# Kernel tuning notes

Measured on AMD Instinct MI355X. Metric: run time of the kernel, lower is better.

The kernel has to match this reference:

```python
import jax, jax.numpy as jnp
import numpy as np

COST_CLASS, COST_MASK, COST_DICE = 2.0, 5.0, 5.0
NUM_POINTS = 12544

def setup_inputs() -> dict:
    key = jax.random.key(0)
    k1, k2, k3, k4, k5 = jax.random.split(key, 5)
    bs, Q, K = 4, 100, 134
    H = W = 256
    M = 80
    P = H * W
    pred_logits = jax.random.normal(k1, (bs, Q, K), dtype=jnp.float32)
    pred_masks = jax.random.normal(k2, (bs, Q, H, W), dtype=jnp.float32)
    tgt_labels = jax.random.randint(k3, (M,), 0, K - 1, dtype=jnp.int32)
    # binary target masks, stored as float (matches .float() in torch code)
    tgt_masks = (jax.random.uniform(k4, (M, H, W)) > 0.5).astype(jnp.float32)
    # random subset of points without replacement (torch.randperm[:num_points])
    point_idx = jax.random.permutation(k5, P)[:NUM_POINTS].astype(jnp.int32)
    return {"pred_logits": pred_logits, "pred_masks": pred_masks,
            "tgt_labels": tgt_labels, "tgt_masks": tgt_masks,
            "point_idx": point_idx}

def reference(pred_logits, pred_masks, tgt_labels, tgt_masks, point_idx):
    bs, Q, K = pred_logits.shape
    N = bs * Q
    M = tgt_masks.shape[0]
    Pn = point_idx.shape[0]

    # class cost: -p[n, tgt_id[m]]
    out_prob = jax.nn.softmax(pred_logits.reshape(N, K), axis=-1)
    tgt_ids = jnp.clip(tgt_labels.astype(jnp.int32), 0, K - 1)
    cost_class = -out_prob[:, tgt_ids]                      # (N, M)

    # sampled mask logits / targets
    x = pred_masks.reshape(N, -1)[:, point_idx]             # (N, Pn) logits
    y = tgt_masks.reshape(M, -1)[:, point_idx]              # (M, Pn) binary float

    # BCE-with-logits cost, separable form:
    # mean_p[softplus(x) - x*y] = mean_p softplus(x) - (x @ y^T)/Pn
    sp_mean = jnp.mean(jax.nn.softplus(x), axis=-1)         # (N,)
    xy = jnp.einsum('np,mp->nm', x, y)                      # (N, M)
    cost_mask = sp_mean[:, None] - xy / Pn

    # dice cost
    s = jax.nn.sigmoid(x)                                   # (N, Pn)
    numer = 2.0 * jnp.einsum('np,mp->nm', s, y)             # (N, M)
    denom = jnp.sum(s, axis=-1)[:, None] + jnp.sum(y, axis=-1)[None, :]
    cost_dice = 1.0 - (numer + 1.0) / (denom + 1.0)

    C = COST_CLASS * cost_class + COST_MASK * cost_mask + COST_DICE * cost_dice
    return C.reshape(bs, Q, M)
```

## Files before the change

### kernel.cpp

```cpp
#include <hip/hip_runtime.h>
#include <math.h>

#define N_ROWS 400
#define M_ROWS 80
#define K_CLS  134
#define PN     12544
#define PFULL  65536
#define NSUB   25
#define TSTEPS 392
#define KSPLIT 98
#define TPB    4

#define GY_BLOCKS 245
#define SM_BLOCKS 50

typedef __attribute__((ext_vector_type(4))) float  f32x4;
typedef __attribute__((ext_vector_type(8))) __bf16 bf16x8;

__device__ __forceinline__ float wave_reduce_sum(float v) {
#pragma unroll
    for (int off = 32; off > 0; off >>= 1) v += __shfl_down(v, off, 64);
    return v;
}

__global__ __launch_bounds__(1024) void sel_sort_kernel(
        const int* __restrict__ point_idx, int* __restrict__ sel,
        float* __restrict__ zero_region, int zero_n) {
    __shared__ unsigned int flagw[PFULL / 4];
    __shared__ int wtot[16], wbase[16];
    int tid = threadIdx.x;
    for (int i = tid; i < PFULL / 4; i += 1024) flagw[i] = 0u;
    for (int i = tid; i < zero_n; i += 1024) zero_region[i] = 0.f;
    __syncthreads();
    unsigned char* flag = (unsigned char*)flagw;
    for (int i = tid; i < PN; i += 1024) flag[point_idx[i]] = 1;
    __syncthreads();
    unsigned int w[16];
    int cnt = 0;
#pragma unroll
    for (int j = 0; j < 16; ++j) {
        w[j] = flagw[tid * 16 + j];
        cnt += (int)((w[j] * 0x01010101u) >> 24);
    }
    int lane = tid & 63, wid = tid >> 6;
    int v = cnt;
#pragma unroll
    for (int off = 1; off < 64; off <<= 1) {
        int u = __shfl_up(v, off, 64);
        if (lane >= off) v += u;
    }
    if (lane == 63) wtot[wid] = v;
    __syncthreads();
    if (tid == 0) {
        int run = 0;
#pragma unroll
        for (int i = 0; i < 16; ++i) { wbase[i] = run; run += wtot[i]; }
    }
    __syncthreads();
    int base = wbase[wid] + (v - cnt);
#pragma unroll
    for (int j = 0; j < 16; ++j) {
        unsigned int u = w[j];
        int p0 = tid * 64 + j * 4;
        if (u & 0x01u)       sel[base++] = p0;
        if (u & 0x0100u)     sel[base++] = p0 + 1;
        if (u & 0x010000u)   sel[base++] = p0 + 2;
        if (u & 0x01000000u) sel[base++] = p0 + 3;
    }
}

__global__ __launch_bounds__(512) void stage1b_kernel(
        const float* __restrict__ tgt_masks, const float* __restrict__ pred_logits,
        const int* __restrict__ sel, __bf16* __restrict__ Yb,
        float* __restrict__ ysum, float* __restrict__ rowmax, float* __restrict__ rowsum) {
    __shared__ float smem[128];
    int b = blockIdx.x;
    if (b < GY_BLOCKS) {
        int j = b / 49, tch = b % 49;
        int wave = threadIdx.x >> 6, lane = threadIdx.x & 63;
        int colL = lane & 15, quad = lane >> 4;
        int m = 16 * j + colL;
        int t = tch * 8 + wave;
        int k0 = t * 32 + quad * 8;
        const float* yrow = tgt_masks + (size_t)m * PFULL;
        int idx[8];
        *(int4*)(idx)     = *(const int4*)(sel + k0);
        *(int4*)(idx + 4) = *(const int4*)(sel + k0 + 4);
        bf16x8 v; float acc = 0.f;
#pragma unroll
        for (int jj = 0; jj < 8; ++jj) {
            float y = yrow[idx[jj]];
            v[jj] = (__bf16)y;
            acc += y;
        }
        ((bf16x8*)Yb)[(size_t)(t * 5 + j) * 64 + lane] = v;
        acc += __shfl_down(acc, 32, 64);
        acc += __shfl_down(acc, 16, 64);
        if (quad == 0) smem[wave * 16 + colL] = acc;
        __syncthreads();
        if (threadIdx.x < 16) {
            float s = 0.f;
#pragma unroll
            for (int wv = 0; wv < 8; ++wv) s += smem[wv * 16 + threadIdx.x];
            atomicAdd(&ysum[16 * j + threadIdx.x], s);
        }
    } else {
        int bb = b - GY_BLOCKS;
        int wave = threadIdx.x >> 6, lane = threadIdx.x & 63;
        int n = bb * 8 + wave;
        const float* row = pred_logits + n * K_CLS;
        float mx = -1e30f;
        for (int k = lane; k < K_CLS; k += 64) mx = fmaxf(mx, row[k]);
#pragma unroll
        for (int off = 32; off > 0; off >>= 1) mx = fmaxf(mx, __shfl_down(mx, off, 64));
        mx = __shfl(mx, 0, 64);
        float se = 0.f;
        for (int k = lane; k < K_CLS; k += 64) se += expf(row[k] - mx);
        se = wave_reduce_sum(se);
        if (lane == 0) { rowmax[n] = mx; rowsum[n] = se; }
    }
}

__global__ __launch_bounds__(256) void gemm_fused_kernel(
        const float* __restrict__ pred_masks, const int* __restrict__ sel,
        const __bf16* __restrict__ Yb,
        float* __restrict__ xyacc, float* __restrict__ syacc,
        float* __restrict__ spsum, float* __restrict__ ssum) {
    int wave = threadIdx.x >> 6, lane = threadIdx.x & 63;
    int flat = blockIdx.x * 4 + wave;
    if (flat >= NSUB * KSPLIT) return;
    int nsub = flat / KSPLIT, kc = flat % KSPLIT;
    int n0 = nsub * 16;
    int colL = lane & 15, quad = lane >> 4;
    int tbase = kc * TPB;

    const float* row = pred_masks + (size_t)(n0 + colL) * PFULL;
    const bf16x8* Yfrag = (const bf16x8*)Yb;

    f32x4 accX[5], accS[5];
    f32x4 zero = {0.f, 0.f, 0.f, 0.f};
#pragma unroll
    for (int j = 0; j < 5; ++j) { accX[j] = zero; accS[j] = zero; }
    float sumS = 0.f, sumSP = 0.f;

    float xs[2][8];
    bf16x8 Bbuf[2][5];
    auto load = [&](int i, int b) {
        int t = tbase + i;
        int k0 = t * 32 + quad * 8;
        int idx[8];
        *(int4*)(idx)     = *(const int4*)(sel + k0);
        *(int4*)(idx + 4) = *(const int4*)(sel + k0 + 4);
#pragma unroll
        for (int jj = 0; jj < 8; ++jj) xs[b][jj] = row[idx[jj]];
        const bf16x8* q = Yfrag + (size_t)(t * 5) * 64 + lane;
#pragma unroll
        for (int j = 0; j < 5; ++j) Bbuf[b][j] = q[(size_t)j * 64];
    };
    auto process = [&](int b) {
        bf16x8 aX, aS;
#pragma unroll
        for (int jj = 0; jj < 8; ++jj) {
            float x  = xs[b][jj];
            float ax = fabsf(x);
            float e  = __expf(-ax);
            float inv = __builtin_amdgcn_rcpf(1.f + e);
            float sig = (x >= 0.f) ? inv : e * inv;
            float sp  = fmaxf(x, 0.f) + __logf(1.f + e);
            aX[jj] = (__bf16)x; aS[jj] = (__bf16)sig;
            sumS += sig; sumSP += sp;
        }
#pragma unroll
        for (int j = 0; j < 5; ++j) {
            accX[j] = __builtin_amdgcn_mfma_f32_16x16x32_bf16(aX, Bbuf[b][j], accX[j], 0, 0, 0);
            accS[j] = __builtin_amdgcn_mfma_f32_16x16x32_bf16(aS, Bbuf[b][j], accS[j], 0, 0, 0);
        }
    };

    load(0, 0);
#pragma unroll
    for (int i = 0; i < TPB; ++i) {
        int b = i & 1;
        if (i + 1 < TPB) load(i + 1, b ^ 1);
        process(b);
    }

#pragma unroll
    for (int j = 0; j < 5; ++j)
#pragma unroll
        for (int r = 0; r < 4; ++r) {
            int n = n0 + quad * 4 + r;
            int m = 16 * j + colL;
            atomicAdd(&xyacc[n * M_ROWS + m], accX[j][r]);
            atomicAdd(&syacc[n * M_ROWS + m], accS[j][r]);
        }
    sumS  += __shfl_down(sumS, 32, 64);
    sumS  += __shfl_down(sumS, 16, 64);
    sumSP += __shfl_down(sumSP, 32, 64);
    sumSP += __shfl_down(sumSP, 16, 64);
    if (lane < 16) {
        atomicAdd(&ssum[n0 + lane], sumS);
        atomicAdd(&spsum[n0 + lane], sumSP);
    }
}

__global__ void combine_kernel(const float* __restrict__ logits,
                               const int* __restrict__ tgt_labels,
                               const float* __restrict__ rowmax,
                               const float* __restrict__ rowsum,
                               const float* __restrict__ spsum,
                               const float* __restrict__ ssum,
                               const float* __restrict__ ysum,
                               const float* __restrict__ xyacc,
                               const float* __restrict__ syacc,
                               float* __restrict__ out) {
    int idx = blockIdx.x * blockDim.x + threadIdx.x;
    if (idx >= N_ROWS * M_ROWS) return;
    int n = idx / M_ROWS, m = idx % M_ROWS;
    int tid = tgt_labels[m];
    tid = min(max(tid, 0), K_CLS - 1);
    float p = expf(logits[n * K_CLS + tid] - rowmax[n]) / rowsum[n];
    float cost_class = -p;
    float cost_mask = (spsum[n] - xyacc[idx]) * (1.0f / PN);
    float cost_dice = 1.f - (2.f * syacc[idx] + 1.f) / (ssum[n] + ysum[m] + 1.f);
    out[idx] = 2.f * cost_class + 5.f * cost_mask + 5.f * cost_dice;
}

extern "C" void kernel_launch(void* const* d_in, const int* in_sizes, int n_in,
                              void* d_out, int out_size, void* d_ws, size_t ws_size,
                              hipStream_t stream) {
    const float* pred_logits = (const float*)d_in[0];
    const float* pred_masks  = (const float*)d_in[1];
    const int*   tgt_labels  = (const int*)d_in[2];
    const float* tgt_masks   = (const float*)d_in[3];
    const int*   point_idx   = (const int*)d_in[4];
    float* out = (float*)d_out;

    char* ws = (char*)d_ws;
    size_t off = 0;
    auto carve = [&](size_t nbytes) {
        char* p = ws + off;
        off += (nbytes + 255) & ~(size_t)255;
        return p;
    };
    float* xyacc = (float*)carve((size_t)N_ROWS * M_ROWS * 4);
    float* syacc = (float*)carve((size_t)N_ROWS * M_ROWS * 4);
    float* ysum  = (float*)carve(M_ROWS * 4);
    float* spsum = (float*)carve(N_ROWS * 4);
    float* ssum  = (float*)carve(N_ROWS * 4);
    int zero_n = (int)(off / 4);
    int*   sel    = (int*)carve(PN * 4);
    float* rowmax = (float*)carve(N_ROWS * 4);
    float* rowsum = (float*)carve(N_ROWS * 4);
    __bf16* Yb = (__bf16*)carve((size_t)TSTEPS * 5 * 1024);
    (void)ws_size; (void)in_sizes; (void)n_in; (void)out_size;

    sel_sort_kernel<<<1, 1024, 0, stream>>>(point_idx, sel, xyacc, zero_n);
    stage1b_kernel<<<GY_BLOCKS + SM_BLOCKS, 512, 0, stream>>>(
        tgt_masks, pred_logits, sel, Yb, ysum, rowmax, rowsum);
    int nwaves = NSUB * KSPLIT;
    gemm_fused_kernel<<<(nwaves + 3) / 4, 256, 0, stream>>>(
        pred_masks, sel, Yb, xyacc, syacc, spsum, ssum);
    combine_kernel<<<(N_ROWS * M_ROWS + 255) / 256, 256, 0, stream>>>(
        pred_logits, tgt_labels, rowmax, rowsum, spsum, ssum, ysum, xyacc, syacc, out);
}
```

Before: 217.7 us.

## Rebalance stages: bitmask sort with softmax, parallel zeroing, finer GEMM K-split

The single-block sort kernel now builds a 65536-bit bitmask with atomicOr and emits indices via popcount/ctz. Softmax row stats move into this launch as extra blocks. Workspace zeroing moves out of the one-block kernel into dedicated vectorized blocks of the gather stage, and per-chunk target sums are written without atomics and summed in the combine kernel. The GEMM K-split doubles to 196 chunks of 2 steps with all loads issued up front. This gives more waves and shorter serial work, at the cost of twice as many output atomics.

```diff
diff --git a/kernel.cpp b/kernel.cpp
--- a/kernel.cpp
+++ b/kernel.cpp
@@ -8,11 +8,11 @@
 #define PFULL  65536
 #define NSUB   25
 #define TSTEPS 392
-#define KSPLIT 98
-#define TPB    4
-
+#define KSPLIT 196
+#define TPB    2
+
+#define ZB_BLOCKS 33
 #define GY_BLOCKS 245
-#define SM_BLOCKS 50
 
 typedef __attribute__((ext_vector_type(4))) float  f32x4;
 typedef __attribute__((ext_vector_type(8))) __bf16 bf16x8;
@@ -23,91 +23,46 @@
     return v;
 }
 
-__global__ __launch_bounds__(1024) void sel_sort_kernel(
+__global__ __launch_bounds__(1024) void sort_softmax_kernel(
         const int* __restrict__ point_idx, int* __restrict__ sel,
-        float* __restrict__ zero_region, int zero_n) {
-    __shared__ unsigned int flagw[PFULL / 4];
-    __shared__ int wtot[16], wbase[16];
+        const float* __restrict__ pred_logits,
+        float* __restrict__ rowmax, float* __restrict__ rowsum) {
     int tid = threadIdx.x;
-    for (int i = tid; i < PFULL / 4; i += 1024) flagw[i] = 0u;
-    for (int i = tid; i < zero_n; i += 1024) zero_region[i] = 0.f;
-    __syncthreads();
-    unsigned char* flag = (unsigned char*)flagw;
-    for (int i = tid; i < PN; i += 1024) flag[point_idx[i]] = 1;
-    __syncthreads();
-    unsigned int w[16];
-    int cnt = 0;
-#pragma unroll
-    for (int j = 0; j < 16; ++j) {
-        w[j] = flagw[tid * 16 + j];
-        cnt += (int)((w[j] * 0x01010101u) >> 24);
-    }
-    int lane = tid & 63, wid = tid >> 6;
-    int v = cnt;
-#pragma unroll
-    for (int off = 1; off < 64; off <<= 1) {
-        int u = __shfl_up(v, off, 64);
-        if (lane >= off) v += u;
-    }
-    if (lane == 63) wtot[wid] = v;
-    __syncthreads();
-    if (tid == 0) {
-        int run = 0;
-#pragma unroll
-        for (int i = 0; i < 16; ++i) { wbase[i] = run; run += wtot[i]; }
-    }
-    __syncthreads();
-    int base = wbase[wid] + (v - cnt);
-#pragma unroll
-    for (int j = 0; j < 16; ++j) {
-        unsigned int u = w[j];
-        int p0 = tid * 64 + j * 4;
-        if (u & 0x01u)       sel[base++] = p0;
-        if (u & 0x0100u)     sel[base++] = p0 + 1;
-        if (u & 0x010000u)   sel[base++] = p0 + 2;
-        if (u & 0x01000000u) sel[base++] = p0 + 3;
-    }
-}
-
-__global__ __launch_bounds__(512) void stage1b_kernel(
-        const float* __restrict__ tgt_masks, const float* __restrict__ pred_logits,
-        const int* __restrict__ sel, __bf16* __restrict__ Yb,
-        float* __restrict__ ysum, float* __restrict__ rowmax, float* __restrict__ rowsum) {
-    __shared__ float smem[128];
-    int b = blockIdx.x;
-    if (b < GY_BLOCKS) {
-        int j = b / 49, tch = b % 49;
-        int wave = threadIdx.x >> 6, lane = threadIdx.x & 63;
-        int colL = lane & 15, quad = lane >> 4;
-        int m = 16 * j + colL;
-        int t = tch * 8 + wave;
-        int k0 = t * 32 + quad * 8;
-        const float* yrow = tgt_masks + (size_t)m * PFULL;
-        int idx[8];
-        *(int4*)(idx)     = *(const int4*)(sel + k0);
-        *(int4*)(idx + 4) = *(const int4*)(sel + k0 + 4);
-        bf16x8 v; float acc = 0.f;
-#pragma unroll
-        for (int jj = 0; jj < 8; ++jj) {
-            float y = yrow[idx[jj]];
-            v[jj] = (__bf16)y;
-            acc += y;
-        }
-        ((bf16x8*)Yb)[(size_t)(t * 5 + j) * 64 + lane] = v;
-        acc += __shfl_down(acc, 32, 64);
-        acc += __shfl_down(acc, 16, 64);
-        if (quad == 0) smem[wave * 16 + colL] = acc;
-        __syncthreads();
-        if (threadIdx.x < 16) {
-            float s = 0.f;
-#pragma unroll
-            for (int wv = 0; wv < 8; ++wv) s += smem[wv * 16 + threadIdx.x];
-            atomicAdd(&ysum[16 * j + threadIdx.x], s);
-        }
+    if (blockIdx.x == 0) {
+        __shared__ unsigned int bits[PFULL / 32];
+        __shared__ int wtot[16], wbase[16];
+        bits[tid] = 0u; bits[tid + 1024] = 0u;
+        __syncthreads();
+        for (int i = tid; i < PN; i += 1024) {
+            int p = point_idx[i];
+            atomicOr(&bits[p >> 5], 1u << (p & 31));
+        }
+        __syncthreads();
+        unsigned int w0 = bits[tid * 2], w1 = bits[tid * 2 + 1];
+        int cnt = __popc(w0) + __popc(w1);
+        int lane = tid & 63, wid = tid >> 6;
+        int v = cnt;
+#pragma unroll
+        for (int off = 1; off < 64; off <<= 1) {
+            int u = __shfl_up(v, off, 64);
+            if (lane >= off) v += u;
+        }
+        if (lane == 63) wtot[wid] = v;
+        __syncthreads();
+        if (tid == 0) {
+            int run = 0;
+#pragma unroll
+            for (int i = 0; i < 16; ++i) { wbase[i] = run; run += wtot[i]; }
+        }
+        __syncthreads();
+        int base = wbase[wid] + (v - cnt);
+        int p0 = tid * 64;
+        while (w0) { int b = __builtin_ctz(w0); w0 &= w0 - 1; sel[base++] = p0 + b; }
+        p0 += 32;
+        while (w1) { int b = __builtin_ctz(w1); w1 &= w1 - 1; sel[base++] = p0 + b; }
     } else {
-        int bb = b - GY_BLOCKS;
-        int wave = threadIdx.x >> 6, lane = threadIdx.x & 63;
-        int n = bb * 8 + wave;
+        int wave = tid >> 6, lane = tid & 63;
+        int n = (blockIdx.x - 1) * 16 + wave;
         const float* row = pred_logits + n * K_CLS;
         float mx = -1e30f;
         for (int k = lane; k < K_CLS; k += 64) mx = fmaxf(mx, row[k]);
@@ -118,6 +73,51 @@
         for (int k = lane; k < K_CLS; k += 64) se += expf(row[k] - mx);
         se = wave_reduce_sum(se);
         if (lane == 0) { rowmax[n] = mx; rowsum[n] = se; }
+    }
+}
+
+__global__ __launch_bounds__(512) void stage1b_kernel(
+        const float* __restrict__ tgt_masks, const int* __restrict__ sel,
+        __bf16* __restrict__ Yb, float* __restrict__ ypart,
+        float* __restrict__ zero_region, int zero_n4) {
+    __shared__ float smem[128];
+    int b = blockIdx.x;
+    if (b < ZB_BLOCKS) {
+        int i = b * 512 + threadIdx.x;
+        if (i < zero_n4) {
+            f32x4 z = {0.f, 0.f, 0.f, 0.f};
+            ((f32x4*)zero_region)[i] = z;
+        }
+        return;
+    }
+    int bb = b - ZB_BLOCKS;
+    int j = bb / 49, tch = bb % 49;
+    int wave = threadIdx.x >> 6, lane = threadIdx.x & 63;
+    int colL = lane & 15, quad = lane >> 4;
+    int m = 16 * j + colL;
+    int t = tch * 8 + wave;
+    int k0 = t * 32 + quad * 8;
+    const float* yrow = tgt_masks + (size_t)m * PFULL;
+    int idx[8];
+    *(int4*)(idx)     = *(const int4*)(sel + k0);
+    *(int4*)(idx + 4) = *(const int4*)(sel + k0 + 4);
+    bf16x8 v; float acc = 0.f;
+#pragma unroll
+    for (int jj = 0; jj < 8; ++jj) {
+        float y = yrow[idx[jj]];
+        v[jj] = (__bf16)y;
+        acc += y;
+    }
+    ((bf16x8*)Yb)[(size_t)(t * 5 + j) * 64 + lane] = v;
+    acc += __shfl_down(acc, 32, 64);
+    acc += __shfl_down(acc, 16, 64);
+    if (quad == 0) smem[wave * 16 + colL] = acc;
+    __syncthreads();
+    if (threadIdx.x < 16) {
+        float s = 0.f;
+#pragma unroll
+        for (int wv = 0; wv < 8; ++wv) s += smem[wv * 16 + threadIdx.x];
+        ypart[tch * M_ROWS + 16 * j + threadIdx.x] = s;
     }
 }
 
@@ -128,7 +128,6 @@
         float* __restrict__ spsum, float* __restrict__ ssum) {
     int wave = threadIdx.x >> 6, lane = threadIdx.x & 63;
     int flat = blockIdx.x * 4 + wave;
-    if (flat >= NSUB * KSPLIT) return;
     int nsub = flat / KSPLIT, kc = flat % KSPLIT;
     int n0 = nsub * 16;
     int colL = lane & 15, quad = lane >> 4;
@@ -143,25 +142,27 @@
     for (int j = 0; j < 5; ++j) { accX[j] = zero; accS[j] = zero; }
     float sumS = 0.f, sumSP = 0.f;
 
-    float xs[2][8];
-    bf16x8 Bbuf[2][5];
-    auto load = [&](int i, int b) {
+    float xs[TPB][8];
+    bf16x8 Bbuf[TPB][5];
+#pragma unroll
+    for (int i = 0; i < TPB; ++i) {
         int t = tbase + i;
         int k0 = t * 32 + quad * 8;
         int idx[8];
         *(int4*)(idx)     = *(const int4*)(sel + k0);
         *(int4*)(idx + 4) = *(const int4*)(sel + k0 + 4);
 #pragma unroll
-        for (int jj = 0; jj < 8; ++jj) xs[b][jj] = row[idx[jj]];
+        for (int jj = 0; jj < 8; ++jj) xs[i][jj] = row[idx[jj]];
         const bf16x8* q = Yfrag + (size_t)(t * 5) * 64 + lane;
 #pragma unroll
-        for (int j = 0; j < 5; ++j) Bbuf[b][j] = q[(size_t)j * 64];
-    };
-    auto process = [&](int b) {
+        for (int j = 0; j < 5; ++j) Bbuf[i][j] = q[(size_t)j * 64];
+    }
+#pragma unroll
+    for (int i = 0; i < TPB; ++i) {
         bf16x8 aX, aS;
 #pragma unroll
         for (int jj = 0; jj < 8; ++jj) {
-            float x  = xs[b][jj];
+            float x  = xs[i][jj];
             float ax = fabsf(x);
             float e  = __expf(-ax);
             float inv = __builtin_amdgcn_rcpf(1.f + e);
@@ -172,17 +173,9 @@
         }
 #pragma unroll
         for (int j = 0; j < 5; ++j) {
-            accX[j] = __builtin_amdgcn_mfma_f32_16x16x32_bf16(aX, Bbuf[b][j], accX[j], 0, 0, 0);
-            accS[j] = __builtin_amdgcn_mfma_f32_16x16x32_bf16(aS, Bbuf[b][j], accS[j], 0, 0, 0);
-        }
-    };
-
-    load(0, 0);
-#pragma unroll
-    for (int i = 0; i < TPB; ++i) {
-        int b = i & 1;
-        if (i + 1 < TPB) load(i + 1, b ^ 1);
-        process(b);
+            accX[j] = __builtin_amdgcn_mfma_f32_16x16x32_bf16(aX, Bbuf[i][j], accX[j], 0, 0, 0);
+            accS[j] = __builtin_amdgcn_mfma_f32_16x16x32_bf16(aS, Bbuf[i][j], accS[j], 0, 0, 0);
+        }
     }
 
 #pragma unroll
@@ -210,19 +203,22 @@
                                const float* __restrict__ rowsum,
                                const float* __restrict__ spsum,
                                const float* __restrict__ ssum,
-                               const float* __restrict__ ysum,
+                               const float* __restrict__ ypart,
                                const float* __restrict__ xyacc,
                                const float* __restrict__ syacc,
                                float* __restrict__ out) {
     int idx = blockIdx.x * blockDim.x + threadIdx.x;
     if (idx >= N_ROWS * M_ROWS) return;
     int n = idx / M_ROWS, m = idx % M_ROWS;
+    float ysum = 0.f;
+#pragma unroll
+    for (int t = 0; t < 49; ++t) ysum += ypart[t * M_ROWS + m];
     int tid = tgt_labels[m];
     tid = min(max(tid, 0), K_CLS - 1);
     float p = expf(logits[n * K_CLS + tid] - rowmax[n]) / rowsum[n];
     float cost_class = -p;
     float cost_mask = (spsum[n] - xyacc[idx]) * (1.0f / PN);
-    float cost_dice = 1.f - (2.f * syacc[idx] + 1.f) / (ssum[n] + ysum[m] + 1.f);
+    float cost_dice = 1.f - (2.f * syacc[idx] + 1.f) / (ssum[n] + ysum + 1.f);
     out[idx] = 2.f * cost_class + 5.f * cost_mask + 5.f * cost_dice;
 }
 
@@ -245,22 +241,21 @@
     };
     float* xyacc = (float*)carve((size_t)N_ROWS * M_ROWS * 4);
     float* syacc = (float*)carve((size_t)N_ROWS * M_ROWS * 4);
-    float* ysum  = (float*)carve(M_ROWS * 4);
     float* spsum = (float*)carve(N_ROWS * 4);
     float* ssum  = (float*)carve(N_ROWS * 4);
-    int zero_n = (int)(off / 4);
+    int zero_n4 = (int)(off / 16);
     int*   sel    = (int*)carve(PN * 4);
     float* rowmax = (float*)carve(N_ROWS * 4);
     float* rowsum = (float*)carve(N_ROWS * 4);
+    float* ypart  = (float*)carve(49 * M_ROWS * 4);
     __bf16* Yb = (__bf16*)carve((size_t)TSTEPS * 5 * 1024);
     (void)ws_size; (void)in_sizes; (void)n_in; (void)out_size;
 
-    sel_sort_kernel<<<1, 1024, 0, stream>>>(point_idx, sel, xyacc, zero_n);
-    stage1b_kernel<<<GY_BLOCKS + SM_BLOCKS, 512, 0, stream>>>(
-        tgt_masks, pred_logits, sel, Yb, ysum, rowmax, rowsum);
-    int nwaves = NSUB * KSPLIT;
-    gemm_fused_kernel<<<(nwaves + 3) / 4, 256, 0, stream>>>(
+    sort_softmax_kernel<<<26, 1024, 0, stream>>>(point_idx, sel, pred_logits, rowmax, rowsum);
+    stage1b_kernel<<<ZB_BLOCKS + GY_BLOCKS, 512, 0, stream>>>(
+        tgt_masks, sel, Yb, ypart, xyacc, zero_n4);
+    gemm_fused_kernel<<<NSUB * KSPLIT / 4, 256, 0, stream>>>(
         pred_masks, sel, Yb, xyacc, syacc, spsum, ssum);
     combine_kernel<<<(N_ROWS * M_ROWS + 255) / 256, 256, 0, stream>>>(
-        pred_logits, tgt_labels, rowmax, rowsum, spsum, ssum, ysum, xyacc, syacc, out);
-}
+        pred_logits, tgt_labels, rowmax, rowsum, spsum, ssum, ypart, xyacc, syacc, out);
+}
```

After: 223.8 us. +2.8%, slower.
